# Kernel tuning notes

Hardware: AMD Instinct MI355X
Metric: run time of the kernel (lower is better)

Reference implementation:

```python
import jax, jax.numpy as jnp
import numpy as np
from jax import lax

T, B, D, H, C = 2048, 64, 128, 256, 5

def setup_inputs() -> dict:
    key = jax.random.key(0)
    k = jax.random.split(key, 7)
    s = 1.0 / np.sqrt(H)  # pytorch nn.RNN init scale
    return {
        "inputs": jax.random.normal(k[0], (T, B, D), dtype=jnp.float32),
        "W_ih": jax.random.uniform(k[1], (H, D), jnp.float32, -s, s),
        "W_hh": jax.random.uniform(k[2], (H, H), jnp.float32, -s, s),
        "b_ih": jax.random.uniform(k[3], (H,), jnp.float32, -s, s),
        "b_hh": jax.random.uniform(k[4], (H,), jnp.float32, -s, s),
        "W_fc": jax.random.uniform(k[5], (C, H), jnp.float32, -s, s),
        "b_fc": jax.random.uniform(k[6], (C,), jnp.float32, -s, s),
    }

def reference(inputs, W_ih, W_hh, b_ih, b_hh, W_fc, b_fc):
    # Precompute input projections for all timesteps: (T, B, H)
    x_proj = jnp.einsum('tbd,hd->tbh', inputs, W_ih) + b_ih + b_hh

    def step(h, xp):
        # h_t = tanh(W_ih x_t + b_ih + W_hh h_{t-1} + b_hh)
        h_new = jnp.tanh(xp + h @ W_hh.T)
        return h_new, None  # per-step outputs unused by the module head

    h0 = jnp.zeros((inputs.shape[1], W_hh.shape[0]), dtype=inputs.dtype)
    h_last, _ = lax.scan(step, h0, x_proj)

    logits = h_last @ W_fc.T + b_fc  # (B, 5)
    return jax.nn.log_softmax(logits, axis=1)
```

## Files before the change

kernel.cpp:

```cpp
#include <hip/hip_runtime.h>


#define T_DIM 2048
#define B_DIM 64
#define D_DIM 128
#define H_DIM 256
#define C_DIM 5

using floatx4 = __attribute__((ext_vector_type(4))) float;
using shortx8 = __attribute__((ext_vector_type(8))) short;
using half4v  = __attribute__((ext_vector_type(4))) _Float16;

#define W_SCALE 2032.0f
#define H_SCALE 127.0f
#define INV_SCALE (1.0f / (2032.0f * 127.0f))

__device__ __forceinline__ short f2bf(float f) {
  unsigned int u = __float_as_uint(f);
  unsigned int r = (u + 0x7FFFu + ((u >> 16) & 1u)) >> 16;
  return (short)r;
}

__device__ __forceinline__ int sdot4(unsigned int a, unsigned int b, int c) {
#if __has_builtin(__builtin_amdgcn_sdot4)
  return __builtin_amdgcn_sdot4((int)a, (int)b, c, false);
#else
  int r = c;
  #pragma unroll
  for (int k = 0; k < 4; ++k)
    r += (int)(signed char)(a >> (8 * k)) * (int)(signed char)(b >> (8 * k));
  return r;
#endif
}

template<int CTRL>
__device__ __forceinline__ int dpp_movi(int x) {
  return __builtin_amdgcn_update_dpp(0, x, CTRL, 0xF, 0xF, true);
}

__device__ __forceinline__ void barrier_lds_only() {
  asm volatile("s_waitcnt lgkmcnt(0)\n\ts_barrier" ::: "memory");
}

#define TS_PER_BLOCK 4
__global__ __launch_bounds__(256) void xp_kernel(
    const float* __restrict__ x,
    const float* __restrict__ W_ih,
    const float* __restrict__ b_ih,
    const float* __restrict__ b_hh,
    _Float16* __restrict__ xp,
    int cnt)
{
  const int tid  = threadIdx.x;
  const int wv   = tid >> 6;
  const int lane = tid & 63;
  const int col  = lane & 15;
  const int quad = lane >> 4;

  shortx8 af[4][4];
  #pragma unroll
  for (int mt = 0; mt < 4; ++mt) {
    const float* wrow = W_ih + (wv * 64 + mt * 16 + col) * D_DIM + quad * 8;
    #pragma unroll
    for (int kf = 0; kf < 4; ++kf) {
      float4 p0 = *(const float4*)(wrow + kf * 32);
      float4 p1 = *(const float4*)(wrow + kf * 32 + 4);
      shortx8 v;
      v[0]=f2bf(p0.x); v[1]=f2bf(p0.y); v[2]=f2bf(p0.z); v[3]=f2bf(p0.w);
      v[4]=f2bf(p1.x); v[5]=f2bf(p1.y); v[6]=f2bf(p1.z); v[7]=f2bf(p1.w);
      af[mt][kf] = v;
    }
  }
  float bias[4][4];
  #pragma unroll
  for (int mt = 0; mt < 4; ++mt)
    #pragma unroll
    for (int r = 0; r < 4; ++r) {
      const int h = wv * 64 + mt * 16 + quad * 4 + r;
      bias[mt][r] = b_ih[h] + b_hh[h];
    }

  for (int tl = 0; tl < TS_PER_BLOCK; ++tl) {
    const int t = blockIdx.x * TS_PER_BLOCK + tl;
    if (t >= cnt) break;
    #pragma unroll
    for (int nt = 0; nt < 4; ++nt) {
      const float* xrow = x + ((long)t * 64 + nt * 16 + col) * D_DIM + quad * 8;
      floatx4 acc[4] = {{0.f,0.f,0.f,0.f},{0.f,0.f,0.f,0.f},
                        {0.f,0.f,0.f,0.f},{0.f,0.f,0.f,0.f}};
      #pragma unroll
      for (int kf = 0; kf < 4; ++kf) {
        float4 p0 = *(const float4*)(xrow + kf * 32);
        float4 p1 = *(const float4*)(xrow + kf * 32 + 4);
        shortx8 bf;
        bf[0]=f2bf(p0.x); bf[1]=f2bf(p0.y); bf[2]=f2bf(p0.z); bf[3]=f2bf(p0.w);
        bf[4]=f2bf(p1.x); bf[5]=f2bf(p1.y); bf[6]=f2bf(p1.z); bf[7]=f2bf(p1.w);
        #pragma unroll
        for (int mt = 0; mt < 4; ++mt)
          acc[mt] = __builtin_amdgcn_mfma_f32_16x16x32_bf16(af[mt][kf], bf, acc[mt], 0, 0, 0);
      }
      _Float16* obase = xp + ((size_t)t * 64 + nt * 16 + col) * H_DIM
                           + wv * 64 + quad * 4;
      #pragma unroll
      for (int mt = 0; mt < 4; ++mt) {
        half4v o;
        o[0] = (_Float16)(acc[mt][0] + bias[mt][0]);
        o[1] = (_Float16)(acc[mt][1] + bias[mt][1]);
        o[2] = (_Float16)(acc[mt][2] + bias[mt][2]);
        o[3] = (_Float16)(acc[mt][3] + bias[mt][3]);
        *(half4v*)(obase + mt * 16) = o;
      }
    }
  }
}

__global__ __launch_bounds__(256)
__attribute__((amdgpu_waves_per_eu(1, 1)))
void scan_kernel(
    const _Float16* __restrict__ xp,
    const float* __restrict__ W_hh,
    const float* __restrict__ W_fc,
    const float* __restrict__ b_fc,
    float* __restrict__ h_state,
    float* __restrict__ out,
    int cnt, int first, int last)
{
  __shared__ __align__(16) signed char hbuf[2][256];
  __shared__ float hfin[H_DIM];
  __shared__ float scratch[192];
  const int b   = blockIdx.x;
  const int tid = threadIdx.x;
  const int g   = tid >> 2;
  const int c   = tid & 3;

  unsigned int wq[4][16];
  const float* wbase = W_hh + (g * 4) * H_DIM + c * 64;
  #pragma unroll
  for (int r = 0; r < 4; ++r)
    #pragma unroll
    for (int i = 0; i < 16; ++i) {
      float4 f = *(const float4*)(wbase + r * H_DIM + i * 4);
      unsigned int q0 = (unsigned int)(int)rintf(f.x * W_SCALE) & 0xFFu;
      unsigned int q1 = (unsigned int)(int)rintf(f.y * W_SCALE) & 0xFFu;
      unsigned int q2 = (unsigned int)(int)rintf(f.z * W_SCALE) & 0xFFu;
      unsigned int q3 = (unsigned int)(int)rintf(f.w * W_SCALE) & 0xFFu;
      wq[r][i] = q0 | (q1 << 8) | (q2 << 16) | (q3 << 24);
    }
  #pragma unroll
  for (int r = 0; r < 4; ++r)
    #pragma unroll
    for (int i = 0; i < 16; ++i)
      asm volatile("" : "+v"(wq[r][i]));

  const int row_w = tid;
  {
    float h0 = first ? 0.f : h_state[b * H_DIM + row_w];
    hbuf[0][row_w] = (signed char)(int)rintf(h0 * H_SCALE);
  }
  __syncthreads();

  const size_t BH = (size_t)B_DIM * H_DIM;
  const _Float16* xpp = xp + (size_t)b * H_DIM + row_w;
  float hnlast = 0.f;

  auto step_body = [&](int bufsel, _Float16 xin) -> void {
    const signed char* hb = hbuf[bufsel] + c * 64;
    uint4 u0 = *(const uint4*)(hb);
    uint4 u1 = *(const uint4*)(hb + 16);
    uint4 u2 = *(const uint4*)(hb + 32);
    uint4 u3 = *(const uint4*)(hb + 48);
    const unsigned int hv[16] = {u0.x, u0.y, u0.z, u0.w, u1.x, u1.y, u1.z, u1.w,
                                 u2.x, u2.y, u2.z, u2.w, u3.x, u3.y, u3.z, u3.w};
    int a0 = 0, a1 = 0, a2 = 0, a3 = 0;
    #pragma unroll
    for (int i = 0; i < 16; ++i) {
      a0 = sdot4(wq[0][i], hv[i], a0);
      a1 = sdot4(wq[1][i], hv[i], a1);
      a2 = sdot4(wq[2][i], hv[i], a2);
      a3 = sdot4(wq[3][i], hv[i], a3);
    }
    int k01 = (c & 1) ? a1 : a0;
    int s01 = (c & 1) ? a0 : a1;
    int m0  = k01 + dpp_movi<0xB1>(s01);
    int k23 = (c & 1) ? a3 : a2;
    int s23 = (c & 1) ? a2 : a3;
    int m1  = k23 + dpp_movi<0xB1>(s23);
    int kk = (c & 2) ? m1 : m0;
    int sn = (c & 2) ? m0 : m1;
    int vi = kk + dpp_movi<0x4E>(sn);

    float p = (float)vi * INV_SCALE + (float)xin;
    float e   = __expf(2.f * p);
    float hqf = 127.f - __fdividef(254.f, e + 1.f);
    hnlast = hqf;
    hbuf[bufsel ^ 1][row_w] = (signed char)(int)rintf(hqf);
    barrier_lds_only();
  };

  if ((cnt & 1) == 0 && cnt >= 2) {
    const _Float16* p = xpp;
    _Float16 x0 = p[0];
    _Float16 x1 = p[BH];
    int s = 0;
    for (; s + 2 < cnt; s += 2) {
      step_body(0, x0); x0 = p[2 * BH];
      step_body(1, x1); x1 = p[3 * BH];
      p += 2 * BH;
    }
    step_body(0, x0);
    step_body(1, x1);
  } else {
    for (int s = 0; s < cnt; ++s)
      step_body(s & 1, xpp[(size_t)s * BH]);
  }

  {
    const float hT = hnlast * (1.0f / 127.0f);
    h_state[b * H_DIM + row_w] = hT;
    hfin[row_w] = hT;
  }

  if (last) {
    __syncthreads();
    if (tid < 160) {
      const int c5 = tid >> 5, i = tid & 31;
      float pp = 0.f;
      #pragma unroll
      for (int jj = 0; jj < 8; ++jj) {
        const int j = i * 8 + jj;
        pp += W_fc[c5 * H_DIM + j] * hfin[j];
      }
      scratch[tid] = pp;
    }
    __syncthreads();
    if (tid < C_DIM) {
      float l = b_fc[tid];
      for (int i = 0; i < 32; ++i) l += scratch[tid * 32 + i];
      scratch[160 + tid] = l;
    }
    __syncthreads();
    if (tid == 0) {
      float mx = scratch[160];
      for (int i = 1; i < C_DIM; ++i) mx = fmaxf(mx, scratch[160 + i]);
      float se = 0.f;
      for (int i = 0; i < C_DIM; ++i) se += __expf(scratch[160 + i] - mx);
      const float lse = mx + __logf(se);
      for (int i = 0; i < C_DIM; ++i) out[b * C_DIM + i] = scratch[160 + i] - lse;
    }
  }
}

extern "C" void kernel_launch(void* const* d_in, const int* in_sizes, int n_in,
                              void* d_out, int out_size, void* d_ws, size_t ws_size,
                              hipStream_t stream) {
  (void)in_sizes; (void)n_in; (void)out_size;
  const float* x    = (const float*)d_in[0];
  const float* W_ih = (const float*)d_in[1];
  const float* W_hh = (const float*)d_in[2];
  const float* b_ih = (const float*)d_in[3];
  const float* b_hh = (const float*)d_in[4];
  const float* W_fc = (const float*)d_in[5];
  const float* b_fc = (const float*)d_in[6];
  float* out = (float*)d_out;

  char* ws = (char*)d_ws;
  float* h_state = (float*)ws;
  _Float16* xp = (_Float16*)(ws + 65536);
  const size_t avail = ws_size > 65536 ? ws_size - 65536 : 0;
  long Tc = (long)(avail / ((size_t)B_DIM * H_DIM * sizeof(_Float16)));
  if (Tc > T_DIM) Tc = T_DIM;
  if (Tc < 1) Tc = 1;

  for (long t0 = 0; t0 < T_DIM; t0 += Tc) {
    const long cnt = (T_DIM - t0 < Tc) ? (T_DIM - t0) : Tc;
    const unsigned xpb = (unsigned)((cnt + TS_PER_BLOCK - 1) / TS_PER_BLOCK);
    xp_kernel<<<dim3(xpb), dim3(256), 0, stream>>>(
        x + t0 * B_DIM * D_DIM, W_ih, b_ih, b_hh, xp, (int)cnt);
    scan_kernel<<<dim3(B_DIM), dim3(256), 0, stream>>>(
        xp, W_hh, W_fc, b_fc, h_state, out,
        (int)cnt, t0 == 0 ? 1 : 0, (t0 + cnt == T_DIM) ? 1 : 0);
  }
}
```

Before: 769.0 us.

## Fuse input projection and recurrent scan into one cooperative kernel

Merges the xp projection kernel and the scan kernel into a single cooperative launch with 64 blocks. Each block first computes its share of timestep projections, staging x through double-buffered LDS as bf16, then all blocks meet at a grid-wide sync before running the recurrence. This drops one kernel launch and the gap between launches per chunk. In exchange the projection phase now runs on only 64 blocks instead of many, and the grid sync adds its own cost.

```diff
diff --git a/kernel.cpp b/kernel.cpp
--- a/kernel.cpp
+++ b/kernel.cpp
@@ -1,4 +1,7 @@
 #include <hip/hip_runtime.h>
+#include <hip/hip_cooperative_groups.h>
+
+namespace cg = cooperative_groups;
 
 
 #define T_DIM 2048
@@ -42,96 +45,120 @@
   asm volatile("s_waitcnt lgkmcnt(0)\n\ts_barrier" ::: "memory");
 }
 
-#define TS_PER_BLOCK 4
-__global__ __launch_bounds__(256) void xp_kernel(
+#define XROW 136
+
+__global__ __launch_bounds__(256)
+__attribute__((amdgpu_waves_per_eu(1, 1)))
+void fused_kernel(
     const float* __restrict__ x,
     const float* __restrict__ W_ih,
+    const float* __restrict__ W_hh,
     const float* __restrict__ b_ih,
     const float* __restrict__ b_hh,
-    _Float16* __restrict__ xp,
-    int cnt)
-{
-  const int tid  = threadIdx.x;
-  const int wv   = tid >> 6;
-  const int lane = tid & 63;
-  const int col  = lane & 15;
-  const int quad = lane >> 4;
-
-  shortx8 af[4][4];
-  #pragma unroll
-  for (int mt = 0; mt < 4; ++mt) {
-    const float* wrow = W_ih + (wv * 64 + mt * 16 + col) * D_DIM + quad * 8;
-    #pragma unroll
-    for (int kf = 0; kf < 4; ++kf) {
-      float4 p0 = *(const float4*)(wrow + kf * 32);
-      float4 p1 = *(const float4*)(wrow + kf * 32 + 4);
-      shortx8 v;
-      v[0]=f2bf(p0.x); v[1]=f2bf(p0.y); v[2]=f2bf(p0.z); v[3]=f2bf(p0.w);
-      v[4]=f2bf(p1.x); v[5]=f2bf(p1.y); v[6]=f2bf(p1.z); v[7]=f2bf(p1.w);
-      af[mt][kf] = v;
-    }
-  }
-  float bias[4][4];
-  #pragma unroll
-  for (int mt = 0; mt < 4; ++mt)
-    #pragma unroll
-    for (int r = 0; r < 4; ++r) {
-      const int h = wv * 64 + mt * 16 + quad * 4 + r;
-      bias[mt][r] = b_ih[h] + b_hh[h];
-    }
-
-  for (int tl = 0; tl < TS_PER_BLOCK; ++tl) {
-    const int t = blockIdx.x * TS_PER_BLOCK + tl;
-    if (t >= cnt) break;
-    #pragma unroll
-    for (int nt = 0; nt < 4; ++nt) {
-      const float* xrow = x + ((long)t * 64 + nt * 16 + col) * D_DIM + quad * 8;
-      floatx4 acc[4] = {{0.f,0.f,0.f,0.f},{0.f,0.f,0.f,0.f},
-                        {0.f,0.f,0.f,0.f},{0.f,0.f,0.f,0.f}};
-      #pragma unroll
-      for (int kf = 0; kf < 4; ++kf) {
-        float4 p0 = *(const float4*)(xrow + kf * 32);
-        float4 p1 = *(const float4*)(xrow + kf * 32 + 4);
-        shortx8 bf;
-        bf[0]=f2bf(p0.x); bf[1]=f2bf(p0.y); bf[2]=f2bf(p0.z); bf[3]=f2bf(p0.w);
-        bf[4]=f2bf(p1.x); bf[5]=f2bf(p1.y); bf[6]=f2bf(p1.z); bf[7]=f2bf(p1.w);
-        #pragma unroll
-        for (int mt = 0; mt < 4; ++mt)
-          acc[mt] = __builtin_amdgcn_mfma_f32_16x16x32_bf16(af[mt][kf], bf, acc[mt], 0, 0, 0);
-      }
-      _Float16* obase = xp + ((size_t)t * 64 + nt * 16 + col) * H_DIM
-                           + wv * 64 + quad * 4;
-      #pragma unroll
-      for (int mt = 0; mt < 4; ++mt) {
-        half4v o;
-        o[0] = (_Float16)(acc[mt][0] + bias[mt][0]);
-        o[1] = (_Float16)(acc[mt][1] + bias[mt][1]);
-        o[2] = (_Float16)(acc[mt][2] + bias[mt][2]);
-        o[3] = (_Float16)(acc[mt][3] + bias[mt][3]);
-        *(half4v*)(obase + mt * 16) = o;
-      }
-    }
-  }
-}
-
-__global__ __launch_bounds__(256)
-__attribute__((amdgpu_waves_per_eu(1, 1)))
-void scan_kernel(
-    const _Float16* __restrict__ xp,
-    const float* __restrict__ W_hh,
     const float* __restrict__ W_fc,
     const float* __restrict__ b_fc,
+    _Float16* __restrict__ xp,
     float* __restrict__ h_state,
     float* __restrict__ out,
     int cnt, int first, int last)
 {
+  __shared__ __align__(16) short xlds[2][64 * XROW];
   __shared__ __align__(16) signed char hbuf[2][256];
   __shared__ float hfin[H_DIM];
   __shared__ float scratch[192];
+
   const int b   = blockIdx.x;
   const int tid = threadIdx.x;
-  const int g   = tid >> 2;
-  const int c   = tid & 3;
+
+  {
+    const int wv   = tid >> 6;
+    const int lane = tid & 63;
+    const int col  = lane & 15;
+    const int quad = lane >> 4;
+
+    const int TSF = (cnt + 63) >> 6;
+    const int t0  = b * TSF;
+    int nts = cnt - t0; if (nts > TSF) nts = TSF;
+
+    auto stage = [&](int ts, short* dst) {
+      const float* src = x + (size_t)ts * (B_DIM * D_DIM);
+      #pragma unroll
+      for (int j = 0; j < 8; ++j) {
+        const int f = (j * 256 + tid) * 4;
+        float4 v = *(const float4*)(src + f);
+        const int row = f >> 7;
+        const int k   = f & 127;
+        unsigned int lo = (unsigned short)f2bf(v.x) |
+                          ((unsigned int)(unsigned short)f2bf(v.y) << 16);
+        unsigned int hi = (unsigned short)f2bf(v.z) |
+                          ((unsigned int)(unsigned short)f2bf(v.w) << 16);
+        int2 pk; pk.x = (int)lo; pk.y = (int)hi;
+        *(int2*)&dst[row * XROW + k] = pk;
+      }
+    };
+
+    if (nts > 0) {
+      shortx8 af[4][4];
+      #pragma unroll
+      for (int mt = 0; mt < 4; ++mt) {
+        const float* wrow = W_ih + (wv * 64 + mt * 16 + col) * D_DIM + quad * 8;
+        #pragma unroll
+        for (int kf = 0; kf < 4; ++kf) {
+          float4 p0 = *(const float4*)(wrow + kf * 32);
+          float4 p1 = *(const float4*)(wrow + kf * 32 + 4);
+          shortx8 v;
+          v[0]=f2bf(p0.x); v[1]=f2bf(p0.y); v[2]=f2bf(p0.z); v[3]=f2bf(p0.w);
+          v[4]=f2bf(p1.x); v[5]=f2bf(p1.y); v[6]=f2bf(p1.z); v[7]=f2bf(p1.w);
+          af[mt][kf] = v;
+        }
+      }
+      float bias[4][4];
+      #pragma unroll
+      for (int mt = 0; mt < 4; ++mt)
+        #pragma unroll
+        for (int r = 0; r < 4; ++r) {
+          const int h = wv * 64 + mt * 16 + quad * 4 + r;
+          bias[mt][r] = b_ih[h] + b_hh[h];
+        }
+
+      stage(t0, xlds[0]);
+      __syncthreads();
+      for (int tl = 0; tl < nts; ++tl) {
+        const int ts = t0 + tl;
+        if (tl + 1 < nts) stage(ts + 1, xlds[(tl + 1) & 1]);
+        const short* xb = xlds[tl & 1];
+        #pragma unroll
+        for (int nt = 0; nt < 4; ++nt) {
+          floatx4 acc[4] = {{0.f,0.f,0.f,0.f},{0.f,0.f,0.f,0.f},
+                            {0.f,0.f,0.f,0.f},{0.f,0.f,0.f,0.f}};
+          #pragma unroll
+          for (int kf = 0; kf < 4; ++kf) {
+            shortx8 bf = *(const shortx8*)&xb[(nt * 16 + col) * XROW + kf * 32 + quad * 8];
+            #pragma unroll
+            for (int mt = 0; mt < 4; ++mt)
+              acc[mt] = __builtin_amdgcn_mfma_f32_16x16x32_bf16(af[mt][kf], bf, acc[mt], 0, 0, 0);
+          }
+          _Float16* obase = xp + ((size_t)ts * 64 + nt * 16 + col) * H_DIM
+                               + wv * 64 + quad * 4;
+          #pragma unroll
+          for (int mt = 0; mt < 4; ++mt) {
+            half4v o;
+            o[0] = (_Float16)(acc[mt][0] + bias[mt][0]);
+            o[1] = (_Float16)(acc[mt][1] + bias[mt][1]);
+            o[2] = (_Float16)(acc[mt][2] + bias[mt][2]);
+            o[3] = (_Float16)(acc[mt][3] + bias[mt][3]);
+            *(half4v*)(obase + mt * 16) = o;
+          }
+        }
+        __syncthreads();
+      }
+    }
+  }
+
+  cg::this_grid().sync();
+
+  const int g = tid >> 2;
+  const int c = tid & 3;
 
   unsigned int wq[4][16];
   const float* wbase = W_hh + (g * 4) * H_DIM + c * 64;
@@ -272,12 +299,16 @@
   if (Tc < 1) Tc = 1;
 
   for (long t0 = 0; t0 < T_DIM; t0 += Tc) {
-    const long cnt = (T_DIM - t0 < Tc) ? (T_DIM - t0) : Tc;
-    const unsigned xpb = (unsigned)((cnt + TS_PER_BLOCK - 1) / TS_PER_BLOCK);
-    xp_kernel<<<dim3(xpb), dim3(256), 0, stream>>>(
-        x + t0 * B_DIM * D_DIM, W_ih, b_ih, b_hh, xp, (int)cnt);
-    scan_kernel<<<dim3(B_DIM), dim3(256), 0, stream>>>(
-        xp, W_hh, W_fc, b_fc, h_state, out,
-        (int)cnt, t0 == 0 ? 1 : 0, (t0 + cnt == T_DIM) ? 1 : 0);
-  }
-}
+    const long cntl = (T_DIM - t0 < Tc) ? (T_DIM - t0) : Tc;
+    const float* xc = x + t0 * B_DIM * D_DIM;
+    int icnt  = (int)cntl;
+    int ifirst = (t0 == 0) ? 1 : 0;
+    int ilast  = (t0 + cntl == T_DIM) ? 1 : 0;
+    void* args[] = { (void*)&xc, (void*)&W_ih, (void*)&W_hh, (void*)&b_ih,
+                     (void*)&b_hh, (void*)&W_fc, (void*)&b_fc,
+                     (void*)&xp, (void*)&h_state, (void*)&out,
+                     (void*)&icnt, (void*)&ifirst, (void*)&ilast };
+    hipLaunchCooperativeKernel((const void*)fused_kernel, dim3(B_DIM),
+                               dim3(256), args, 0, stream);
+  }
+}
```

Result: slower. 831.8 us (+8.2%).
